# Optimization experiments

Measured on AMD Instinct MI355X. Metric: run time of the kernel, lower is better.

Reference implementation:

```python
import jax, jax.numpy as jnp
import numpy as np

SEQ_LEN = 8192
HIDDEN = 4096
QMAX = 127.0


def _quantize(x_f, scale):
    # per-position requant: round(x / scale), clip to int8 range
    return jnp.clip(jnp.round(x_f / scale[:, None]), -QMAX, QMAX)


def setup_inputs() -> dict:
    key = jax.random.key(0)
    k1, k2, k3, k4 = jax.random.split(key, 4)
    # int8-valued input in [-127, 127]
    x = jax.random.randint(k1, (SEQ_LEN, HIDDEN), -127, 128, dtype=jnp.int32).astype(jnp.int8)
    # per-position scales (calibrated buffers); small positive values typical of int8 activations
    scale_x = jax.random.uniform(k2, (SEQ_LEN,), jnp.float32, 0.01, 0.05)
    scale_y = jax.random.uniform(k3, (SEQ_LEN,), jnp.float32, 0.005, 0.01)  # sigmoid out in (0,1)
    scale_out = jax.random.uniform(k4, (SEQ_LEN,), jnp.float32, 0.01, 0.05)
    return {"x": x, "scale_x": scale_x, "scale_y": scale_y, "scale_out": scale_out}


def reference(x, scale_x, scale_y, scale_out):
    # Quantized SiLU: dequant -> sigmoid -> requant -> dequant both -> mul -> requant
    x_f = x.astype(jnp.float32) * scale_x[:, None]          # [S, H] dequant x
    y_q = _quantize(jax.nn.sigmoid(x_f), scale_y)            # int8-valued sigmoid output
    y_f = y_q * scale_y[:, None]                             # dequant sigmoid output
    out_f = x_f * y_f                                        # elementwise mul in float
    out_q = _quantize(out_f, scale_out).astype(jnp.int8)     # requant to int8
    return out_q, scale_out
```

## Files before the change

### kernel.cpp

```cpp
#include <hip/hip_runtime.h>


#define SEQ_LEN 8192
#define HIDDEN  4096
#define QMAX_F  127.0f
#define THREADS 256
#define VECS_PER_THREAD 4

typedef int   iv4 __attribute__((ext_vector_type(4)));
typedef float fv4 __attribute__((ext_vector_type(4)));

__device__ __forceinline__ float silu_q_one(int xi, float s_x, float s_y,
                                            float r_o) {
    float xf  = (float)xi * s_x;
    float e   = expf(-xf);
    float sig = 1.0f / (1.0f + e);
    float yq  = rintf(sig / s_y);
    yq        = fminf(fmaxf(yq, -QMAX_F), QMAX_F);
    float yf  = yq * s_y;
    float of  = xf * yf;
    float oq  = rintf(of * r_o);
    return fminf(fmaxf(oq, -QMAX_F), QMAX_F);
}

__global__ __launch_bounds__(THREADS) void silu_quant_kernel(
    const int*   __restrict__ x,
    const float* __restrict__ scale_x,
    const float* __restrict__ scale_y,
    const float* __restrict__ scale_out,
    float*       __restrict__ out)
{
    const int row = blockIdx.x;

    const float s_x = scale_x[row];
    const float s_y = scale_y[row];
    const float s_o = scale_out[row];
    const float r_o = 1.0f / s_o;

    const iv4* __restrict__ xrow = (const iv4*)(x + (size_t)row * HIDDEN);
    fv4*       __restrict__ orow = (fv4*)(out + (size_t)row * HIDDEN);

    #pragma unroll
    for (int k = 0; k < VECS_PER_THREAD; ++k) {
        const int v = threadIdx.x + k * THREADS;
        iv4 xv = __builtin_nontemporal_load(xrow + v);
        fv4 o;
        o.x = silu_q_one(xv.x, s_x, s_y, r_o);
        o.y = silu_q_one(xv.y, s_x, s_y, r_o);
        o.z = silu_q_one(xv.z, s_x, s_y, r_o);
        o.w = silu_q_one(xv.w, s_x, s_y, r_o);
        __builtin_nontemporal_store(o, orow + v);
    }

    if (threadIdx.x == 0)
        out[(size_t)SEQ_LEN * HIDDEN + row] = s_o;
}

extern "C" void kernel_launch(void* const* d_in, const int* in_sizes, int n_in,
                              void* d_out, int out_size, void* d_ws, size_t ws_size,
                              hipStream_t stream) {
    const int*   x         = (const int*)  d_in[0];
    const float* scale_x   = (const float*)d_in[1];
    const float* scale_y   = (const float*)d_in[2];
    const float* scale_out = (const float*)d_in[3];
    float*       out       = (float*)d_out;

    silu_quant_kernel<<<SEQ_LEN, THREADS, 0, stream>>>(
        x, scale_x, scale_y, scale_out, out);
}
```

Measured before the change: 226.5 us.

## Replace per-element quantized SiLU with per-row 255-entry LDS lookup table

New measurement: 225.8 us. No clear change (-0.3%).

```diff
diff --git a/kernel.cpp b/kernel.cpp
--- a/kernel.cpp
+++ b/kernel.cpp
@@ -5,7 +5,10 @@
 #define HIDDEN  4096
 #define QMAX_F  127.0f
 #define THREADS 256
-#define VECS_PER_THREAD 4
+#define VPT     4
+#define ROWS_PB 4
+#define NBLOCKS (SEQ_LEN / ROWS_PB)
+#define ROW_V   (HIDDEN / 4)
 
 typedef int   iv4 __attribute__((ext_vector_type(4)));
 typedef float fv4 __attribute__((ext_vector_type(4)));
@@ -30,30 +33,67 @@
     const float* __restrict__ scale_out,
     float*       __restrict__ out)
 {
-    const int row = blockIdx.x;
+    __shared__ float lut[ROWS_PB][256];
 
-    const float s_x = scale_x[row];
-    const float s_y = scale_y[row];
-    const float s_o = scale_out[row];
-    const float r_o = 1.0f / s_o;
+    const int r0 = blockIdx.x * ROWS_PB;
+    const int t  = threadIdx.x;
 
-    const iv4* __restrict__ xrow = (const iv4*)(x + (size_t)row * HIDDEN);
-    fv4*       __restrict__ orow = (fv4*)(out + (size_t)row * HIDDEN);
+    float sx[ROWS_PB], sy[ROWS_PB], so[ROWS_PB], ro[ROWS_PB];
+    #pragma unroll
+    for (int r = 0; r < ROWS_PB; ++r) {
+        sx[r] = scale_x[r0 + r];
+        sy[r] = scale_y[r0 + r];
+        so[r] = scale_out[r0 + r];
+        ro[r] = 1.0f / so[r];
+    }
+
+    const iv4* __restrict__ xrow0 = (const iv4*)(x + (size_t)r0 * HIDDEN);
+    fv4*       __restrict__ orow0 = (fv4*)(out + (size_t)r0 * HIDDEN);
+
+    iv4 xb[2][VPT];
 
     #pragma unroll
-    for (int k = 0; k < VECS_PER_THREAD; ++k) {
-        const int v = threadIdx.x + k * THREADS;
-        iv4 xv = __builtin_nontemporal_load(xrow + v);
-        fv4 o;
-        o.x = silu_q_one(xv.x, s_x, s_y, r_o);
-        o.y = silu_q_one(xv.y, s_x, s_y, r_o);
-        o.z = silu_q_one(xv.z, s_x, s_y, r_o);
-        o.w = silu_q_one(xv.w, s_x, s_y, r_o);
-        __builtin_nontemporal_store(o, orow + v);
+    for (int k = 0; k < VPT; ++k)
+        xb[0][k] = __builtin_nontemporal_load(xrow0 + t + k * THREADS);
+
+    if (t < 255) {
+        #pragma unroll
+        for (int r = 0; r < ROWS_PB; ++r)
+            lut[r][t] = silu_q_one(t - 127, sx[r], sy[r], ro[r]);
     }
 
-    if (threadIdx.x == 0)
-        out[(size_t)SEQ_LEN * HIDDEN + row] = s_o;
+    if (t == 255) {
+        #pragma unroll
+        for (int r = 0; r < ROWS_PB; ++r)
+            out[(size_t)SEQ_LEN * HIDDEN + r0 + r] = so[r];
+    }
+
+    __syncthreads();
+
+    #pragma unroll
+    for (int r = 0; r < ROWS_PB; ++r) {
+        const int cur = r & 1;
+
+        if (r + 1 < ROWS_PB) {
+            #pragma unroll
+            for (int k = 0; k < VPT; ++k)
+                xb[cur ^ 1][k] = __builtin_nontemporal_load(
+                    xrow0 + (size_t)(r + 1) * ROW_V + t + k * THREADS);
+        }
+
+        const float* lutc = &lut[r][127];
+        #pragma unroll
+        for (int k = 0; k < VPT; ++k) {
+            iv4 xv = xb[cur][k];
+            fv4 o;
+            o.x = lutc[xv.x];
+            o.y = lutc[xv.y];
+            o.z = lutc[xv.z];
+            o.w = lutc[xv.w];
+            __builtin_nontemporal_store(
+                o, orow0 + (size_t)r * ROW_V + t + k * THREADS);
+        }
+    }
 }
 
 extern "C" void kernel_launch(void* const* d_in, const int* in_sizes, int n_in,
@@ -65,6 +105,6 @@
     const float* scale_out = (const float*)d_in[3];
     float*       out       = (float*)d_out;
 
-    silu_quant_kernel<<<SEQ_LEN, THREADS, 0, stream>>>(
+    silu_quant_kernel<<<NBLOCKS, THREADS, 0, stream>>>(
         x, scale_x, scale_y, scale_out, out);
 }
```
